# Performance work log

Hardware: AMD Instinct MI355X
Metric: run time of the kernel (lower is better)

## Reference

```python
import jax, jax.numpy as jnp
import numpy as np

N = 50000   # nodes
E = 800000  # edges (avg degree 16)
IN = 128    # in_feats
D = 64      # h_feats
H = 4       # n_heads
NEG_SLOPE = 0.2  # DGL GATConv default leaky_relu slope
L = 3       # n_layers (conv_hs)


def setup_inputs() -> dict:
    key = jax.random.key(0)
    ks = jax.random.split(key, 16)
    s = 0.05
    inp = {
        "in_feat": jax.random.normal(ks[0], (N, IN), jnp.float32),
        "src": jax.random.randint(ks[1], (E,), 0, N),
        "dst": jax.random.randint(ks[2], (E,), 0, N),
        # conv1 params (DGL GATConv: fc no bias, attn_l/attn_r, output bias)
        "W1": jax.random.normal(ks[3], (IN, H * D), jnp.float32) * s,
        "al1": jax.random.normal(ks[4], (H, D), jnp.float32) * s,
        "ar1": jax.random.normal(ks[5], (H, D), jnp.float32) * s,
        "b1": jnp.zeros((H * D,), jnp.float32),
        # stacked hidden GATConv params (L layers)
        "Wh": jax.random.normal(ks[6], (L, D, H * D), jnp.float32) * s,
        "alh": jax.random.normal(ks[7], (L, H, D), jnp.float32) * s,
        "arh": jax.random.normal(ks[8], (L, H, D), jnp.float32) * s,
        "bh": jnp.zeros((L, H * D), jnp.float32),
        # out_ln: Linear(H*D -> D)
        "Wo": jax.random.normal(ks[9], (H * D, D), jnp.float32) * s,
        "bo": jnp.zeros((D,), jnp.float32),
    }
    return inp


def gat_conv(h, W, al, ar, b, src, dst):
    # h: [N, F_in] -> feat: [N, H, D]
    feat = (h @ W).reshape(N, H, -1)
    el = jnp.einsum('nhd,hd->nh', feat, al)  # [N, H]
    er = jnp.einsum('nhd,hd->nh', feat, ar)  # [N, H]
    e = jax.nn.leaky_relu(el[src] + er[dst], NEG_SLOPE)  # [E, H]
    # segment softmax over incoming edges of each dst node
    emax = jax.ops.segment_max(e, dst, num_segments=N)
    emax = jnp.where(jnp.isfinite(emax), emax, 0.0)  # guard empty segments
    a = jnp.exp(e - emax[dst])
    ssum = jax.ops.segment_sum(a, dst, num_segments=N)
    alpha = a / ssum[dst]  # [E, H]
    # weighted scatter-aggregate of source features
    out = jax.ops.segment_sum(feat[src] * alpha[:, :, None], dst, num_segments=N)
    return out + b.reshape(1, H, -1)  # [N, H, D]


def reference(in_feat, src, dst, W1, al1, ar1, b1, Wh, alh, arh, bh, Wo, bo):
    h = gat_conv(in_feat, W1, al1, ar1, b1, src, dst).mean(axis=1)  # [N, D]
    for i in range(L - 1):
        h = gat_conv(h, Wh[i], alh[i], arh[i], bh[i], src, dst).mean(axis=1)
    h = gat_conv(h, Wh[L - 1], alh[L - 1], arh[L - 1], bh[L - 1], src, dst)  # [N, H, D]
    h = h.reshape(N, H * D) @ Wo + bo  # [N, D]
    # LayerNorm(elementwise_affine=False)
    mu = h.mean(axis=-1, keepdims=True)
    var = ((h - mu) ** 2).mean(axis=-1, keepdims=True)
    return (h - mu) / jnp.sqrt(var + 1e-5)
```

## Files before the change

### kernel.cpp

```cpp
#include <hip/hip_runtime.h>

#define NN 50000
#define NE 800000

__device__ __forceinline__ float wsum64(float v) {
#pragma unroll
  for (int off = 32; off; off >>= 1) v += __shfl_xor(v, off, 64);
  return v;
}
__device__ __forceinline__ float lrelu(float x) { return x > 0.0f ? x : 0.2f * x; }

__global__ void zero_int_k(int* __restrict__ p, int n) {
  int i = blockIdx.x * 256 + threadIdx.x;
  if (i < n) p[i] = 0;
}

__global__ void count_deg_k(const int* __restrict__ dst, int* __restrict__ deg) {
  int e = blockIdx.x * 256 + threadIdx.x;
  if (e < NE) atomicAdd(&deg[dst[e]], 1);
}

__global__ __launch_bounds__(1024) void scan_k(const int* __restrict__ deg,
                                               int* __restrict__ row_ptr,
                                               int* __restrict__ cursor) {
  __shared__ int woff[16];
  int tid = threadIdx.x;
  int lane = tid & 63, wv = tid >> 6;
  const int CH = (NN + 1023) / 1024;
  int lo = tid * CH;
  int hi = lo + CH;
  if (lo > NN) lo = NN;
  if (hi > NN) hi = NN;
  int s = 0;
  for (int i = lo; i < hi; ++i) s += deg[i];
  int incl = s;
#pragma unroll
  for (int off = 1; off < 64; off <<= 1) {
    int t = __shfl_up(incl, off, 64);
    if (lane >= off) incl += t;
  }
  if (lane == 63) woff[wv] = incl;
  __syncthreads();
  if (tid == 0) {
    int run = 0;
#pragma unroll
    for (int w = 0; w < 16; ++w) { int t = woff[w]; woff[w] = run; run += t; }
    row_ptr[NN] = run;
  }
  __syncthreads();
  int run = incl - s + woff[wv];
  for (int i = lo; i < hi; ++i) {
    row_ptr[i] = run;
    cursor[i] = run;
    run += deg[i];
  }
}

__global__ void fill_csr_k(const int* __restrict__ src, const int* __restrict__ dst,
                           int* __restrict__ cursor, int* __restrict__ csr_src) {
  int e = blockIdx.x * 256 + threadIdx.x;
  if (e < NE) {
    int pos = atomicAdd(&cursor[dst[e]], 1);
    csr_src[pos] = src[e];
  }
}

__global__ void compute_q_k(const float* __restrict__ W, const float* __restrict__ al,
                            const float* __restrict__ ar, float* __restrict__ Q, int KDIM) {
  int idx = blockIdx.x * 256 + threadIdx.x;
  if (idx >= KDIM * 8) return;
  int k = idx >> 3, c = idx & 7;
  int h = c & 3;
  const float* av = (c < 4 ? al : ar) + h * 64;
  const float* wrow = W + (size_t)k * 256 + h * 64;
  float s = 0.0f;
  for (int m = 0; m < 64; ++m) s += wrow[m] * av[m];
  Q[idx] = s;
}

__global__ void compute_m_k(const float* __restrict__ Wh2, const float* __restrict__ Wo,
                            float* __restrict__ M) {
  int row = blockIdx.x;
  int d = threadIdx.x;
  int h = row >> 6, k = row & 63;
  float s = 0.0f;
  for (int j = 0; j < 64; ++j)
    s += Wh2[k * 256 + h * 64 + j] * Wo[(h * 64 + j) * 64 + d];
  M[row * 64 + d] = s;
}

__global__ void compute_c_k(const float* __restrict__ bh2, const float* __restrict__ Wo,
                            const float* __restrict__ bo, float* __restrict__ cvec) {
  int d = threadIdx.x;
  if (d >= 64) return;
  float s = bo[d];
  for (int m = 0; m < 256; ++m) s += bh2[m] * Wo[m * 64 + d];
  cvec[d] = s;
}

__global__ __launch_bounds__(256) void eler_l1_k(const float* __restrict__ X,
                                                 const float* __restrict__ Q,
                                                 float* __restrict__ elp,
                                                 float* __restrict__ erp) {
  int n = __builtin_amdgcn_readfirstlane(blockIdx.x * 4 + (threadIdx.x >> 6));
  int lane = threadIdx.x & 63;
  float2 xv = *(const float2*)&X[(n << 7) + (lane << 1)];
  float4 qa0 = *(const float4*)&Q[(lane * 2) * 8];
  float4 qb0 = *(const float4*)&Q[(lane * 2) * 8 + 4];
  float4 qa1 = *(const float4*)&Q[(lane * 2 + 1) * 8];
  float4 qb1 = *(const float4*)&Q[(lane * 2 + 1) * 8 + 4];
  float p[8];
  p[0] = xv.x * qa0.x + xv.y * qa1.x; p[1] = xv.x * qa0.y + xv.y * qa1.y;
  p[2] = xv.x * qa0.z + xv.y * qa1.z; p[3] = xv.x * qa0.w + xv.y * qa1.w;
  p[4] = xv.x * qb0.x + xv.y * qb1.x; p[5] = xv.x * qb0.y + xv.y * qb1.y;
  p[6] = xv.x * qb0.z + xv.y * qb1.z; p[7] = xv.x * qb0.w + xv.y * qb1.w;
#pragma unroll
  for (int c = 0; c < 8; ++c) p[c] = wsum64(p[c]);
  if (lane == 0) {
    *(float4*)&elp[n << 2] = make_float4(p[0], p[1], p[2], p[3]);
    *(float4*)&erp[n << 2] = make_float4(p[4], p[5], p[6], p[7]);
  }
}

__global__ __launch_bounds__(256) void fused_hidden_k(
    const float* __restrict__ x, const float* __restrict__ el,
    const float* __restrict__ er, const float* __restrict__ W,
    const float* __restrict__ b, const float* __restrict__ Qn,
    const int* __restrict__ row_ptr, const int* __restrict__ csr_src,
    float* __restrict__ hout, float* __restrict__ eln, float* __restrict__ ern) {
  __shared__ float gs[4 * 4 * 256];
  int wave = threadIdx.x >> 6, lane = threadIdx.x & 63;
  int q = lane >> 4, r = lane & 15;
  int base = (blockIdx.x * 4 + wave) * 4;
  float* gw = &gs[wave * 1024];
  int r4 = r << 2;
#pragma unroll 1
  for (int t = 0; t < 4; ++t) {
    int n = __builtin_amdgcn_readfirstlane(base + t);
    int beg = row_ptr[n], end = row_ptr[n + 1];
    float erq = er[(n << 2) + q];
    float4 a = make_float4(0.f, 0.f, 0.f, 0.f);
    float sw = 0.f;
#define ESTEP(elv, xv)                      \
  do {                                      \
    float w = __expf(lrelu((elv) + erq));   \
    sw += w;                                \
    a.x = fmaf(w, (xv).x, a.x);             \
    a.y = fmaf(w, (xv).y, a.y);             \
    a.z = fmaf(w, (xv).z, a.z);             \
    a.w = fmaf(w, (xv).w, a.w);             \
  } while (0)
    int j = beg;
    for (; j + 8 <= end; j += 8) {
      int s0 = csr_src[j + 0], s1 = csr_src[j + 1];
      int s2 = csr_src[j + 2], s3 = csr_src[j + 3];
      int s4 = csr_src[j + 4], s5 = csr_src[j + 5];
      int s6 = csr_src[j + 6], s7 = csr_src[j + 7];
      float e0 = el[(s0 << 2) + q], e1 = el[(s1 << 2) + q];
      float e2 = el[(s2 << 2) + q], e3 = el[(s3 << 2) + q];
      float e4 = el[(s4 << 2) + q], e5 = el[(s5 << 2) + q];
      float e6 = el[(s6 << 2) + q], e7 = el[(s7 << 2) + q];
      float4 x0 = *(const float4*)&x[(s0 << 6) + r4];
      float4 x1 = *(const float4*)&x[(s1 << 6) + r4];
      float4 x2 = *(const float4*)&x[(s2 << 6) + r4];
      float4 x3 = *(const float4*)&x[(s3 << 6) + r4];
      float4 x4 = *(const float4*)&x[(s4 << 6) + r4];
      float4 x5 = *(const float4*)&x[(s5 << 6) + r4];
      float4 x6 = *(const float4*)&x[(s6 << 6) + r4];
      float4 x7 = *(const float4*)&x[(s7 << 6) + r4];
      ESTEP(e0, x0); ESTEP(e1, x1); ESTEP(e2, x2); ESTEP(e3, x3);
      ESTEP(e4, x4); ESTEP(e5, x5); ESTEP(e6, x6); ESTEP(e7, x7);
    }
    for (; j < end; ++j) {
      int s0 = csr_src[j];
      float e0 = el[(s0 << 2) + q];
      float4 x0 = *(const float4*)&x[(s0 << 6) + r4];
      ESTEP(e0, x0);
    }
#undef ESTEP
    float inv = sw > 0.f ? 1.0f / sw : 0.f;
    *(float4*)&gw[t * 256 + (q << 6) + r4] =
        make_float4(a.x * inv, a.y * inv, a.z * inv, a.w * inv);
  }
  float y0 = 0.f, y1 = 0.f, y2 = 0.f, y3 = 0.f;
  for (int rr = 0; rr < 256; rr += 4) {
#pragma unroll
    for (int u = 0; u < 4; ++u) {
      int row = rr + u;
      int h = row >> 6, k = row & 63;
      float sv = W[k * 256 + (h << 6) + lane];
      y0 = fmaf(gw[0 * 256 + row], sv, y0);
      y1 = fmaf(gw[1 * 256 + row], sv, y1);
      y2 = fmaf(gw[2 * 256 + row], sv, y2);
      y3 = fmaf(gw[3 * 256 + row], sv, y3);
    }
  }
  float bsum = b[lane] + b[64 + lane] + b[128 + lane] + b[192 + lane];
  float4 qa = *(const float4*)&Qn[lane * 8];
  float4 qb = *(const float4*)&Qn[lane * 8 + 4];
  float ys[4] = {y0, y1, y2, y3};
#pragma unroll
  for (int t = 0; t < 4; ++t) {
    int n = base + t;
    float yv = 0.25f * (ys[t] + bsum);
    hout[(n << 6) + lane] = yv;
    float e0 = wsum64(yv * qa.x), e1 = wsum64(yv * qa.y);
    float e2 = wsum64(yv * qa.z), e3 = wsum64(yv * qa.w);
    float r0 = wsum64(yv * qb.x), r1 = wsum64(yv * qb.y);
    float r2 = wsum64(yv * qb.z), r3 = wsum64(yv * qb.w);
    if (lane == 0) {
      *(float4*)&eln[n << 2] = make_float4(e0, e1, e2, e3);
      *(float4*)&ern[n << 2] = make_float4(r0, r1, r2, r3);
    }
  }
}

__global__ __launch_bounds__(256) void fused_l1_k(
    const float* __restrict__ x, const float* __restrict__ el,
    const float* __restrict__ er, const float* __restrict__ W,
    const float* __restrict__ b, const float* __restrict__ Qn,
    const int* __restrict__ row_ptr, const int* __restrict__ csr_src,
    float* __restrict__ hout, float* __restrict__ eln, float* __restrict__ ern) {
  __shared__ float gs[4 * 4 * 512];
  int wave = threadIdx.x >> 6, lane = threadIdx.x & 63;
  int q = lane >> 4, r = lane & 15;
  int base = (blockIdx.x * 4 + wave) * 4;
  float* gw = &gs[wave * 2048];
  int r8 = r << 3;
#pragma unroll 1
  for (int t = 0; t < 4; ++t) {
    int n = __builtin_amdgcn_readfirstlane(base + t);
    int beg = row_ptr[n], end = row_ptr[n + 1];
    float erq = er[(n << 2) + q];
    float4 aA = make_float4(0.f, 0.f, 0.f, 0.f);
    float4 aB = make_float4(0.f, 0.f, 0.f, 0.f);
    float sw = 0.f;
#define ESTEP(elv, xa, xb)                  \
  do {                                      \
    float w = __expf(lrelu((elv) + erq));   \
    sw += w;                                \
    aA.x = fmaf(w, (xa).x, aA.x);           \
    aA.y = fmaf(w, (xa).y, aA.y);           \
    aA.z = fmaf(w, (xa).z, aA.z);           \
    aA.w = fmaf(w, (xa).w, aA.w);           \
    aB.x = fmaf(w, (xb).x, aB.x);           \
    aB.y = fmaf(w, (xb).y, aB.y);           \
    aB.z = fmaf(w, (xb).z, aB.z);           \
    aB.w = fmaf(w, (xb).w, aB.w);           \
  } while (0)
    int j = beg;
    for (; j + 4 <= end; j += 4) {
      int s0 = csr_src[j + 0], s1 = csr_src[j + 1];
      int s2 = csr_src[j + 2], s3 = csr_src[j + 3];
      float e0 = el[(s0 << 2) + q], e1 = el[(s1 << 2) + q];
      float e2 = el[(s2 << 2) + q], e3 = el[(s3 << 2) + q];
      float4 xa0 = *(const float4*)&x[(s0 << 7) + r8];
      float4 xb0 = *(const float4*)&x[(s0 << 7) + r8 + 4];
      float4 xa1 = *(const float4*)&x[(s1 << 7) + r8];
      float4 xb1 = *(const float4*)&x[(s1 << 7) + r8 + 4];
      float4 xa2 = *(const float4*)&x[(s2 << 7) + r8];
      float4 xb2 = *(const float4*)&x[(s2 << 7) + r8 + 4];
      float4 xa3 = *(const float4*)&x[(s3 << 7) + r8];
      float4 xb3 = *(const float4*)&x[(s3 << 7) + r8 + 4];
      ESTEP(e0, xa0, xb0); ESTEP(e1, xa1, xb1);
      ESTEP(e2, xa2, xb2); ESTEP(e3, xa3, xb3);
    }
    for (; j < end; ++j) {
      int s0 = csr_src[j];
      float e0 = el[(s0 << 2) + q];
      float4 xa0 = *(const float4*)&x[(s0 << 7) + r8];
      float4 xb0 = *(const float4*)&x[(s0 << 7) + r8 + 4];
      ESTEP(e0, xa0, xb0);
    }
#undef ESTEP
    float inv = sw > 0.f ? 1.0f / sw : 0.f;
    *(float4*)&gw[t * 512 + (q << 7) + r8] =
        make_float4(aA.x * inv, aA.y * inv, aA.z * inv, aA.w * inv);
    *(float4*)&gw[t * 512 + (q << 7) + r8 + 4] =
        make_float4(aB.x * inv, aB.y * inv, aB.z * inv, aB.w * inv);
  }
  float y0 = 0.f, y1 = 0.f, y2 = 0.f, y3 = 0.f;
  for (int rr = 0; rr < 512; rr += 4) {
#pragma unroll
    for (int u = 0; u < 4; ++u) {
      int row = rr + u;
      int h = row >> 7, k = row & 127;
      float sv = W[k * 256 + (h << 6) + lane];
      y0 = fmaf(gw[0 * 512 + row], sv, y0);
      y1 = fmaf(gw[1 * 512 + row], sv, y1);
      y2 = fmaf(gw[2 * 512 + row], sv, y2);
      y3 = fmaf(gw[3 * 512 + row], sv, y3);
    }
  }
  float bsum = b[lane] + b[64 + lane] + b[128 + lane] + b[192 + lane];
  float4 qa = *(const float4*)&Qn[lane * 8];
  float4 qb = *(const float4*)&Qn[lane * 8 + 4];
  float ys[4] = {y0, y1, y2, y3};
#pragma unroll
  for (int t = 0; t < 4; ++t) {
    int n = base + t;
    float yv = 0.25f * (ys[t] + bsum);
    hout[(n << 6) + lane] = yv;
    float e0 = wsum64(yv * qa.x), e1 = wsum64(yv * qa.y);
    float e2 = wsum64(yv * qa.z), e3 = wsum64(yv * qa.w);
    float r0 = wsum64(yv * qb.x), r1 = wsum64(yv * qb.y);
    float r2 = wsum64(yv * qb.z), r3 = wsum64(yv * qb.w);
    if (lane == 0) {
      *(float4*)&eln[n << 2] = make_float4(e0, e1, e2, e3);
      *(float4*)&ern[n << 2] = make_float4(r0, r1, r2, r3);
    }
  }
}

__global__ __launch_bounds__(256) void fused_final_k(
    const float* __restrict__ x, const float* __restrict__ el,
    const float* __restrict__ er, const float* __restrict__ M,
    const float* __restrict__ cvec, const int* __restrict__ row_ptr,
    const int* __restrict__ csr_src, float* __restrict__ out) {
  __shared__ float gs[4 * 4 * 256];
  int wave = threadIdx.x >> 6, lane = threadIdx.x & 63;
  int q = lane >> 4, r = lane & 15;
  int base = (blockIdx.x * 4 + wave) * 4;
  float* gw = &gs[wave * 1024];
  int r4 = r << 2;
#pragma unroll 1
  for (int t = 0; t < 4; ++t) {
    int n = __builtin_amdgcn_readfirstlane(base + t);
    int beg = row_ptr[n], end = row_ptr[n + 1];
    float erq = er[(n << 2) + q];
    float4 a = make_float4(0.f, 0.f, 0.f, 0.f);
    float sw = 0.f;
#define ESTEP(elv, xv)                      \
  do {                                      \
    float w = __expf(lrelu((elv) + erq));   \
    sw += w;                                \
    a.x = fmaf(w, (xv).x, a.x);             \
    a.y = fmaf(w, (xv).y, a.y);             \
    a.z = fmaf(w, (xv).z, a.z);             \
    a.w = fmaf(w, (xv).w, a.w);             \
  } while (0)
    int j = beg;
    for (; j + 8 <= end; j += 8) {
      int s0 = csr_src[j + 0], s1 = csr_src[j + 1];
      int s2 = csr_src[j + 2], s3 = csr_src[j + 3];
      int s4 = csr_src[j + 4], s5 = csr_src[j + 5];
      int s6 = csr_src[j + 6], s7 = csr_src[j + 7];
      float e0 = el[(s0 << 2) + q], e1 = el[(s1 << 2) + q];
      float e2 = el[(s2 << 2) + q], e3 = el[(s3 << 2) + q];
      float e4 = el[(s4 << 2) + q], e5 = el[(s5 << 2) + q];
      float e6 = el[(s6 << 2) + q], e7 = el[(s7 << 2) + q];
      float4 x0 = *(const float4*)&x[(s0 << 6) + r4];
      float4 x1 = *(const float4*)&x[(s1 << 6) + r4];
      float4 x2 = *(const float4*)&x[(s2 << 6) + r4];
      float4 x3 = *(const float4*)&x[(s3 << 6) + r4];
      float4 x4 = *(const float4*)&x[(s4 << 6) + r4];
      float4 x5 = *(const float4*)&x[(s5 << 6) + r4];
      float4 x6 = *(const float4*)&x[(s6 << 6) + r4];
      float4 x7 = *(const float4*)&x[(s7 << 6) + r4];
      ESTEP(e0, x0); ESTEP(e1, x1); ESTEP(e2, x2); ESTEP(e3, x3);
      ESTEP(e4, x4); ESTEP(e5, x5); ESTEP(e6, x6); ESTEP(e7, x7);
    }
    for (; j < end; ++j) {
      int s0 = csr_src[j];
      float e0 = el[(s0 << 2) + q];
      float4 x0 = *(const float4*)&x[(s0 << 6) + r4];
      ESTEP(e0, x0);
    }
#undef ESTEP
    float inv = sw > 0.f ? 1.0f / sw : 0.f;
    *(float4*)&gw[t * 256 + (q << 6) + r4] =
        make_float4(a.x * inv, a.y * inv, a.z * inv, a.w * inv);
  }
  float y0 = 0.f, y1 = 0.f, y2 = 0.f, y3 = 0.f;
  for (int rr = 0; rr < 256; rr += 4) {
#pragma unroll
    for (int u = 0; u < 4; ++u) {
      int row = rr + u;
      float sv = M[(row << 6) + lane];
      y0 = fmaf(gw[0 * 256 + row], sv, y0);
      y1 = fmaf(gw[1 * 256 + row], sv, y1);
      y2 = fmaf(gw[2 * 256 + row], sv, y2);
      y3 = fmaf(gw[3 * 256 + row], sv, y3);
    }
  }
  float cl = cvec[lane];
  float ys[4] = {y0 + cl, y1 + cl, y2 + cl, y3 + cl};
#pragma unroll
  for (int t = 0; t < 4; ++t) {
    int n = base + t;
    float y = ys[t];
    float mu = wsum64(y) * (1.0f / 64.0f);
    float dv = y - mu;
    float var = wsum64(dv * dv) * (1.0f / 64.0f);
    out[(n << 6) + lane] = dv * rsqrtf(var + 1e-5f);
  }
}

extern "C" void kernel_launch(void* const* d_in, const int* in_sizes, int n_in,
                              void* d_out, int out_size, void* d_ws, size_t ws_size,
                              hipStream_t stream) {
  const float* in_feat = (const float*)d_in[0];
  const int* src = (const int*)d_in[1];
  const int* dst = (const int*)d_in[2];
  const float* W1 = (const float*)d_in[3];
  const float* al1 = (const float*)d_in[4];
  const float* ar1 = (const float*)d_in[5];
  const float* b1 = (const float*)d_in[6];
  const float* Wh = (const float*)d_in[7];
  const float* alh = (const float*)d_in[8];
  const float* arh = (const float*)d_in[9];
  const float* bh = (const float*)d_in[10];
  const float* Wo = (const float*)d_in[11];
  const float* bo = (const float*)d_in[12];
  float* out = (float*)d_out;

  char* ws = (char*)d_ws;
  size_t off = 0;
  auto alloc = [&](size_t bytes) {
    void* p = ws + off;
    off = (off + bytes + 255) & ~(size_t)255;
    return p;
  };
  float* h_a = (float*)alloc((size_t)NN * 64 * 4);
  float* h_b = (float*)alloc((size_t)NN * 64 * 4);
  float* el_a = (float*)alloc((size_t)NN * 4 * 4);
  float* er_a = (float*)alloc((size_t)NN * 4 * 4);
  float* el_b = (float*)alloc((size_t)NN * 4 * 4);
  float* er_b = (float*)alloc((size_t)NN * 4 * 4);
  float* Q1 = (float*)alloc(128 * 8 * 4);
  float* Q2 = (float*)alloc(64 * 8 * 4);
  float* Q3 = (float*)alloc(64 * 8 * 4);
  float* Q4 = (float*)alloc(64 * 8 * 4);
  float* M = (float*)alloc(256 * 64 * 4);
  float* cvec = (float*)alloc(64 * 4);
  int* deg = (int*)alloc((size_t)NN * 4);
  int* row_ptr = (int*)alloc((size_t)(NN + 1) * 4);
  int* cursor = (int*)alloc((size_t)NN * 4);
  int* csr_src = (int*)alloc((size_t)NE * 4);
  (void)ws_size; (void)in_sizes; (void)n_in; (void)out_size;

  zero_int_k<<<(NN + 255) / 256, 256, 0, stream>>>(deg, NN);
  count_deg_k<<<(NE + 255) / 256, 256, 0, stream>>>(dst, deg);
  scan_k<<<1, 1024, 0, stream>>>(deg, row_ptr, cursor);
  fill_csr_k<<<(NE + 255) / 256, 256, 0, stream>>>(src, dst, cursor, csr_src);

  compute_q_k<<<4, 256, 0, stream>>>(W1, al1, ar1, Q1, 128);
  compute_q_k<<<2, 256, 0, stream>>>(Wh + 0 * 64 * 256, alh + 0 * 256, arh + 0 * 256, Q2, 64);
  compute_q_k<<<2, 256, 0, stream>>>(Wh + 1 * 64 * 256, alh + 1 * 256, arh + 1 * 256, Q3, 64);
  compute_q_k<<<2, 256, 0, stream>>>(Wh + 2 * 64 * 256, alh + 2 * 256, arh + 2 * 256, Q4, 64);
  compute_m_k<<<256, 64, 0, stream>>>(Wh + 2 * 64 * 256, Wo, M);
  compute_c_k<<<1, 64, 0, stream>>>(bh + 2 * 256, Wo, bo, cvec);

  const int FUSED_GRID = NN / 16;
  const int ELER_GRID = NN / 4;

  eler_l1_k<<<ELER_GRID, 256, 0, stream>>>(in_feat, Q1, el_a, er_a);
  fused_l1_k<<<FUSED_GRID, 256, 0, stream>>>(in_feat, el_a, er_a, W1, b1, Q2,
                                             row_ptr, csr_src, h_a, el_b, er_b);
  fused_hidden_k<<<FUSED_GRID, 256, 0, stream>>>(h_a, el_b, er_b, Wh + 0 * 64 * 256,
                                                 bh + 0 * 256, Q3, row_ptr, csr_src,
                                                 h_b, el_a, er_a);
  fused_hidden_k<<<FUSED_GRID, 256, 0, stream>>>(h_b, el_a, er_a, Wh + 1 * 64 * 256,
                                                 bh + 1 * 256, Q4, row_ptr, csr_src,
                                                 h_a, el_b, er_b);
  fused_final_k<<<FUSED_GRID, 256, 0, stream>>>(h_a, el_b, er_b, M, cvec,
                                                row_ptr, csr_src, out);
}
```

Measured before the change: 658.3 us.

## Compute edge softmax weights per chunk in parallel and stage them in LDS

```diff
diff --git a/kernel.cpp b/kernel.cpp
--- a/kernel.cpp
+++ b/kernel.cpp
@@ -9,6 +9,7 @@
   return v;
 }
 __device__ __forceinline__ float lrelu(float x) { return x > 0.0f ? x : 0.2f * x; }
+#define RFL(v) __builtin_amdgcn_readfirstlane(v)
 
 __global__ void zero_int_k(int* __restrict__ p, int n) {
   int i = blockIdx.x * 256 + threadIdx.x;
@@ -102,7 +103,7 @@
                                                  const float* __restrict__ Q,
                                                  float* __restrict__ elp,
                                                  float* __restrict__ erp) {
-  int n = __builtin_amdgcn_readfirstlane(blockIdx.x * 4 + (threadIdx.x >> 6));
+  int n = RFL(blockIdx.x * 4 + (threadIdx.x >> 6));
   int lane = threadIdx.x & 63;
   float2 xv = *(const float2*)&X[(n << 7) + (lane << 1)];
   float4 qa0 = *(const float4*)&Q[(lane * 2) * 8];
@@ -122,65 +123,95 @@
   }
 }
 
+__device__ __forceinline__ void weights_chunk(const float* __restrict__ el,
+                                              const float4& er4,
+                                              const int* __restrict__ csr_src,
+                                              int j0, int cnt, int lane,
+                                              int* __restrict__ s_l,
+                                              float4* __restrict__ w_l,
+                                              float& sw0, float& sw1,
+                                              float& sw2, float& sw3) {
+  float4 wv = make_float4(0.f, 0.f, 0.f, 0.f);
+  int sv = 0;
+  if (lane < cnt) {
+    sv = csr_src[j0 + lane];
+    float4 l4 = *(const float4*)&el[sv << 2];
+    wv.x = __expf(lrelu(l4.x + er4.x));
+    wv.y = __expf(lrelu(l4.y + er4.y));
+    wv.z = __expf(lrelu(l4.z + er4.z));
+    wv.w = __expf(lrelu(l4.w + er4.w));
+  }
+  s_l[lane] = sv;
+  w_l[lane] = wv;
+  sw0 += wsum64(wv.x);
+  sw1 += wsum64(wv.y);
+  sw2 += wsum64(wv.z);
+  sw3 += wsum64(wv.w);
+}
+
 __global__ __launch_bounds__(256) void fused_hidden_k(
     const float* __restrict__ x, const float* __restrict__ el,
     const float* __restrict__ er, const float* __restrict__ W,
     const float* __restrict__ b, const float* __restrict__ Qn,
     const int* __restrict__ row_ptr, const int* __restrict__ csr_src,
     float* __restrict__ hout, float* __restrict__ eln, float* __restrict__ ern) {
-  __shared__ float gs[4 * 4 * 256];
+  __shared__ float gs[4][1024];
+  __shared__ int s_lds[4][64];
+  __shared__ float4 w_lds[4][64];
   int wave = threadIdx.x >> 6, lane = threadIdx.x & 63;
-  int q = lane >> 4, r = lane & 15;
   int base = (blockIdx.x * 4 + wave) * 4;
-  float* gw = &gs[wave * 1024];
-  int r4 = r << 2;
+  float* gw = gs[wave];
+  int* s_l = s_lds[wave];
+  float4* w_l = w_lds[wave];
 #pragma unroll 1
   for (int t = 0; t < 4; ++t) {
-    int n = __builtin_amdgcn_readfirstlane(base + t);
+    int n = RFL(base + t);
     int beg = row_ptr[n], end = row_ptr[n + 1];
-    float erq = er[(n << 2) + q];
-    float4 a = make_float4(0.f, 0.f, 0.f, 0.f);
-    float sw = 0.f;
-#define ESTEP(elv, xv)                      \
-  do {                                      \
-    float w = __expf(lrelu((elv) + erq));   \
-    sw += w;                                \
-    a.x = fmaf(w, (xv).x, a.x);             \
-    a.y = fmaf(w, (xv).y, a.y);             \
-    a.z = fmaf(w, (xv).z, a.z);             \
-    a.w = fmaf(w, (xv).w, a.w);             \
+    float4 er4 = *(const float4*)&er[n << 2];
+    float a0 = 0.f, a1 = 0.f, a2 = 0.f, a3 = 0.f;
+    float sw0 = 0.f, sw1 = 0.f, sw2 = 0.f, sw3 = 0.f;
+#pragma unroll 1
+    for (int j0 = beg; j0 < end; j0 += 64) {
+      int cnt = min(64, end - j0);
+      weights_chunk(el, er4, csr_src, j0, cnt, lane, s_l, w_l, sw0, sw1, sw2, sw3);
+      int j = 0;
+      for (; j + 8 <= cnt; j += 8) {
+        int t0 = RFL(s_l[j + 0]), t1 = RFL(s_l[j + 1]);
+        int t2 = RFL(s_l[j + 2]), t3 = RFL(s_l[j + 3]);
+        int t4 = RFL(s_l[j + 4]), t5 = RFL(s_l[j + 5]);
+        int t6 = RFL(s_l[j + 6]), t7 = RFL(s_l[j + 7]);
+        float x0 = x[(t0 << 6) + lane], x1 = x[(t1 << 6) + lane];
+        float x2 = x[(t2 << 6) + lane], x3 = x[(t3 << 6) + lane];
+        float x4 = x[(t4 << 6) + lane], x5 = x[(t5 << 6) + lane];
+        float x6 = x[(t6 << 6) + lane], x7 = x[(t7 << 6) + lane];
+#define FMA4(Q, X)                                 \
+  do {                                             \
+    float4 qq = (Q);                               \
+    a0 = fmaf(qq.x, (X), a0);                      \
+    a1 = fmaf(qq.y, (X), a1);                      \
+    a2 = fmaf(qq.z, (X), a2);                      \
+    a3 = fmaf(qq.w, (X), a3);                      \
   } while (0)
-    int j = beg;
-    for (; j + 8 <= end; j += 8) {
-      int s0 = csr_src[j + 0], s1 = csr_src[j + 1];
-      int s2 = csr_src[j + 2], s3 = csr_src[j + 3];
-      int s4 = csr_src[j + 4], s5 = csr_src[j + 5];
-      int s6 = csr_src[j + 6], s7 = csr_src[j + 7];
-      float e0 = el[(s0 << 2) + q], e1 = el[(s1 << 2) + q];
-      float e2 = el[(s2 << 2) + q], e3 = el[(s3 << 2) + q];
-      float e4 = el[(s4 << 2) + q], e5 = el[(s5 << 2) + q];
-      float e6 = el[(s6 << 2) + q], e7 = el[(s7 << 2) + q];
-      float4 x0 = *(const float4*)&x[(s0 << 6) + r4];
-      float4 x1 = *(const float4*)&x[(s1 << 6) + r4];
-      float4 x2 = *(const float4*)&x[(s2 << 6) + r4];
-      float4 x3 = *(const float4*)&x[(s3 << 6) + r4];
-      float4 x4 = *(const float4*)&x[(s4 << 6) + r4];
-      float4 x5 = *(const float4*)&x[(s5 << 6) + r4];
-      float4 x6 = *(const float4*)&x[(s6 << 6) + r4];
-      float4 x7 = *(const float4*)&x[(s7 << 6) + r4];
-      ESTEP(e0, x0); ESTEP(e1, x1); ESTEP(e2, x2); ESTEP(e3, x3);
-      ESTEP(e4, x4); ESTEP(e5, x5); ESTEP(e6, x6); ESTEP(e7, x7);
-    }
-    for (; j < end; ++j) {
-      int s0 = csr_src[j];
-      float e0 = el[(s0 << 2) + q];
-      float4 x0 = *(const float4*)&x[(s0 << 6) + r4];
-      ESTEP(e0, x0);
-    }
-#undef ESTEP
-    float inv = sw > 0.f ? 1.0f / sw : 0.f;
-    *(float4*)&gw[t * 256 + (q << 6) + r4] =
-        make_float4(a.x * inv, a.y * inv, a.z * inv, a.w * inv);
+        FMA4(w_l[j + 0], x0); FMA4(w_l[j + 1], x1);
+        FMA4(w_l[j + 2], x2); FMA4(w_l[j + 3], x3);
+        FMA4(w_l[j + 4], x4); FMA4(w_l[j + 5], x5);
+        FMA4(w_l[j + 6], x6); FMA4(w_l[j + 7], x7);
+      }
+      for (; j < cnt; ++j) {
+        int t0 = RFL(s_l[j]);
+        float x0 = x[(t0 << 6) + lane];
+        FMA4(w_l[j], x0);
+      }
+#undef FMA4
+    }
+    float i0 = sw0 > 0.f ? 1.0f / sw0 : 0.f;
+    float i1 = sw1 > 0.f ? 1.0f / sw1 : 0.f;
+    float i2 = sw2 > 0.f ? 1.0f / sw2 : 0.f;
+    float i3 = sw3 > 0.f ? 1.0f / sw3 : 0.f;
+    gw[t * 256 + 0 * 64 + lane] = a0 * i0;
+    gw[t * 256 + 1 * 64 + lane] = a1 * i1;
+    gw[t * 256 + 2 * 64 + lane] = a2 * i2;
+    gw[t * 256 + 3 * 64 + lane] = a3 * i3;
   }
   float y0 = 0.f, y1 = 0.f, y2 = 0.f, y3 = 0.f;
   for (int rr = 0; rr < 256; rr += 4) {
@@ -221,63 +252,73 @@
     const float* __restrict__ b, const float* __restrict__ Qn,
     const int* __restrict__ row_ptr, const int* __restrict__ csr_src,
     float* __restrict__ hout, float* __restrict__ eln, float* __restrict__ ern) {
-  __shared__ float gs[4 * 4 * 512];
+  __shared__ float gs[4][2048];
+  __shared__ int s_lds[4][64];
+  __shared__ float4 w_lds[4][64];
   int wave = threadIdx.x >> 6, lane = threadIdx.x & 63;
-  int q = lane >> 4, r = lane & 15;
   int base = (blockIdx.x * 4 + wave) * 4;
-  float* gw = &gs[wave * 2048];
-  int r8 = r << 3;
+  float* gw = gs[wave];
+  int* s_l = s_lds[wave];
+  float4* w_l = w_lds[wave];
+  int lane2 = lane << 1;
 #pragma unroll 1
   for (int t = 0; t < 4; ++t) {
-    int n = __builtin_amdgcn_readfirstlane(base + t);
+    int n = RFL(base + t);
     int beg = row_ptr[n], end = row_ptr[n + 1];
-    float erq = er[(n << 2) + q];
-    float4 aA = make_float4(0.f, 0.f, 0.f, 0.f);
-    float4 aB = make_float4(0.f, 0.f, 0.f, 0.f);
-    float sw = 0.f;
-#define ESTEP(elv, xa, xb)                  \
-  do {                                      \
-    float w = __expf(lrelu((elv) + erq));   \
-    sw += w;                                \
-    aA.x = fmaf(w, (xa).x, aA.x);           \
-    aA.y = fmaf(w, (xa).y, aA.y);           \
-    aA.z = fmaf(w, (xa).z, aA.z);           \
-    aA.w = fmaf(w, (xa).w, aA.w);           \
-    aB.x = fmaf(w, (xb).x, aB.x);           \
-    aB.y = fmaf(w, (xb).y, aB.y);           \
-    aB.z = fmaf(w, (xb).z, aB.z);           \
-    aB.w = fmaf(w, (xb).w, aB.w);           \
+    float4 er4 = *(const float4*)&er[n << 2];
+    float a0x = 0.f, a0y = 0.f, a1x = 0.f, a1y = 0.f;
+    float a2x = 0.f, a2y = 0.f, a3x = 0.f, a3y = 0.f;
+    float sw0 = 0.f, sw1 = 0.f, sw2 = 0.f, sw3 = 0.f;
+#pragma unroll 1
+    for (int j0 = beg; j0 < end; j0 += 64) {
+      int cnt = min(64, end - j0);
+      weights_chunk(el, er4, csr_src, j0, cnt, lane, s_l, w_l, sw0, sw1, sw2, sw3);
+      int j = 0;
+      for (; j + 8 <= cnt; j += 8) {
+        int t0 = RFL(s_l[j + 0]), t1 = RFL(s_l[j + 1]);
+        int t2 = RFL(s_l[j + 2]), t3 = RFL(s_l[j + 3]);
+        int t4 = RFL(s_l[j + 4]), t5 = RFL(s_l[j + 5]);
+        int t6 = RFL(s_l[j + 6]), t7 = RFL(s_l[j + 7]);
+        float2 x0 = *(const float2*)&x[(t0 << 7) + lane2];
+        float2 x1 = *(const float2*)&x[(t1 << 7) + lane2];
+        float2 x2 = *(const float2*)&x[(t2 << 7) + lane2];
+        float2 x3 = *(const float2*)&x[(t3 << 7) + lane2];
+        float2 x4 = *(const float2*)&x[(t4 << 7) + lane2];
+        float2 x5 = *(const float2*)&x[(t5 << 7) + lane2];
+        float2 x6 = *(const float2*)&x[(t6 << 7) + lane2];
+        float2 x7 = *(const float2*)&x[(t7 << 7) + lane2];
+#define FMA8(Q, X)                                   \
+  do {                                               \
+    float4 qq = (Q);                                 \
+    a0x = fmaf(qq.x, (X).x, a0x);                    \
+    a0y = fmaf(qq.x, (X).y, a0y);                    \
+    a1x = fmaf(qq.y, (X).x, a1x);                    \
+    a1y = fmaf(qq.y, (X).y, a1y);                    \
+    a2x = fmaf(qq.z, (X).x, a2x);                    \
+    a2y = fmaf(qq.z, (X).y, a2y);                    \
+    a3x = fmaf(qq.w, (X).x, a3x);                    \
+    a3y = fmaf(qq.w, (X).y, a3y);                    \
   } while (0)
-    int j = beg;
-    for (; j + 4 <= end; j += 4) {
-      int s0 = csr_src[j + 0], s1 = csr_src[j + 1];
-      int s2 = csr_src[j + 2], s3 = csr_src[j + 3];
-      float e0 = el[(s0 << 2) + q], e1 = el[(s1 << 2) + q];
-      float e2 = el[(s2 << 2) + q], e3 = el[(s3 << 2) + q];
-      float4 xa0 = *(const float4*)&x[(s0 << 7) + r8];
-      float4 xb0 = *(const float4*)&x[(s0 << 7) + r8 + 4];
-      float4 xa1 = *(const float4*)&x[(s1 << 7) + r8];
-      float4 xb1 = *(const float4*)&x[(s1 << 7) + r8 + 4];
-      float4 xa2 = *(const float4*)&x[(s2 << 7) + r8];
-      float4 xb2 = *(const float4*)&x[(s2 << 7) + r8 + 4];
-      float4 xa3 = *(const float4*)&x[(s3 << 7) + r8];
-      float4 xb3 = *(const float4*)&x[(s3 << 7) + r8 + 4];
-      ESTEP(e0, xa0, xb0); ESTEP(e1, xa1, xb1);
-      ESTEP(e2, xa2, xb2); ESTEP(e3, xa3, xb3);
-    }
-    for (; j < end; ++j) {
-      int s0 = csr_src[j];
-      float e0 = el[(s0 << 2) + q];
-      float4 xa0 = *(const float4*)&x[(s0 << 7) + r8];
-      float4 xb0 = *(const float4*)&x[(s0 << 7) + r8 + 4];
-      ESTEP(e0, xa0, xb0);
-    }
-#undef ESTEP
-    float inv = sw > 0.f ? 1.0f / sw : 0.f;
-    *(float4*)&gw[t * 512 + (q << 7) + r8] =
-        make_float4(aA.x * inv, aA.y * inv, aA.z * inv, aA.w * inv);
-    *(float4*)&gw[t * 512 + (q << 7) + r8 + 4] =
-        make_float4(aB.x * inv, aB.y * inv, aB.z * inv, aB.w * inv);
+        FMA8(w_l[j + 0], x0); FMA8(w_l[j + 1], x1);
+        FMA8(w_l[j + 2], x2); FMA8(w_l[j + 3], x3);
+        FMA8(w_l[j + 4], x4); FMA8(w_l[j + 5], x5);
+        FMA8(w_l[j + 6], x6); FMA8(w_l[j + 7], x7);
+      }
+      for (; j < cnt; ++j) {
+        int t0 = RFL(s_l[j]);
+        float2 x0 = *(const float2*)&x[(t0 << 7) + lane2];
+        FMA8(w_l[j], x0);
+      }
+#undef FMA8
+    }
+    float i0 = sw0 > 0.f ? 1.0f / sw0 : 0.f;
+    float i1 = sw1 > 0.f ? 1.0f / sw1 : 0.f;
+    float i2 = sw2 > 0.f ? 1.0f / sw2 : 0.f;
+    float i3 = sw3 > 0.f ? 1.0f / sw3 : 0.f;
+    *(float2*)&gw[t * 512 + 0 * 128 + lane2] = make_float2(a0x * i0, a0y * i0);
+    *(float2*)&gw[t * 512 + 1 * 128 + lane2] = make_float2(a1x * i1, a1y * i1);
+    *(float2*)&gw[t * 512 + 2 * 128 + lane2] = make_float2(a2x * i2, a2y * i2);
+    *(float2*)&gw[t * 512 + 3 * 128 + lane2] = make_float2(a3x * i3, a3y * i3);
   }
   float y0 = 0.f, y1 = 0.f, y2 = 0.f, y3 = 0.f;
   for (int rr = 0; rr < 512; rr += 4) {
@@ -317,59 +358,63 @@
     const float* __restrict__ er, const float* __restrict__ M,
     const float* __restrict__ cvec, const int* __restrict__ row_ptr,
     const int* __restrict__ csr_src, float* __restrict__ out) {
-  __shared__ float gs[4 * 4 * 256];
+  __shared__ float gs[4][1024];
+  __shared__ int s_lds[4][64];
+  __shared__ float4 w_lds[4][64];
   int wave = threadIdx.x >> 6, lane = threadIdx.x & 63;
-  int q = lane >> 4, r = lane & 15;
   int base = (blockIdx.x * 4 + wave) * 4;
-  float* gw = &gs[wave * 1024];
-  int r4 = r << 2;
+  float* gw = gs[wave];
+  int* s_l = s_lds[wave];
+  float4* w_l = w_lds[wave];
 #pragma unroll 1
   for (int t = 0; t < 4; ++t) {
-    int n = __builtin_amdgcn_readfirstlane(base + t);
+    int n = RFL(base + t);
     int beg = row_ptr[n], end = row_ptr[n + 1];
-    float erq = er[(n << 2) + q];
-    float4 a = make_float4(0.f, 0.f, 0.f, 0.f);
-    float sw = 0.f;
-#define ESTEP(elv, xv)                      \
-  do {                                      \
-    float w = __expf(lrelu((elv) + erq));   \
-    sw += w;                                \
-    a.x = fmaf(w, (xv).x, a.x);             \
-    a.y = fmaf(w, (xv).y, a.y);             \
-    a.z = fmaf(w, (xv).z, a.z);             \
-    a.w = fmaf(w, (xv).w, a.w);             \
+    float4 er4 = *(const float4*)&er[n << 2];
+    float a0 = 0.f, a1 = 0.f, a2 = 0.f, a3 = 0.f;
+    float sw0 = 0.f, sw1 = 0.f, sw2 = 0.f, sw3 = 0.f;
+#pragma unroll 1
+    for (int j0 = beg; j0 < end; j0 += 64) {
+      int cnt = min(64, end - j0);
+      weights_chunk(el, er4, csr_src, j0, cnt, lane, s_l, w_l, sw0, sw1, sw2, sw3);
+      int j = 0;
+      for (; j + 8 <= cnt; j += 8) {
+        int t0 = RFL(s_l[j + 0]), t1 = RFL(s_l[j + 1]);
+        int t2 = RFL(s_l[j + 2]), t3 = RFL(s_l[j + 3]);
+        int t4 = RFL(s_l[j + 4]), t5 = RFL(s_l[j + 5]);
+        int t6 = RFL(s_l[j + 6]), t7 = RFL(s_l[j + 7]);
+        float x0 = x[(t0 << 6) + lane], x1 = x[(t1 << 6) + lane];
+        float x2 = x[(t2 << 6) + lane], x3 = x[(t3 << 6) + lane];
+        float x4 = x[(t4 << 6) + lane], x5 = x[(t5 << 6) + lane];
+        float x6 = x[(t6 << 6) + lane], x7 = x[(t7 << 6) + lane];
+#define FMA4(Q, X)                                 \
+  do {                                             \
+    float4 qq = (Q);                               \
+    a0 = fmaf(qq.x, (X), a0);                      \
+    a1 = fmaf(qq.y, (X), a1);                      \
+    a2 = fmaf(qq.z, (X), a2);                      \
+    a3 = fmaf(qq.w, (X), a3);                      \
   } while (0)
-    int j = beg;
-    for (; j + 8 <= end; j += 8) {
-      int s0 = csr_src[j + 0], s1 = csr_src[j + 1];
-      int s2 = csr_src[j + 2], s3 = csr_src[j + 3];
-      int s4 = csr_src[j + 4], s5 = csr_src[j + 5];
-      int s6 = csr_src[j + 6], s7 = csr_src[j + 7];
-      float e0 = el[(s0 << 2) + q], e1 = el[(s1 << 2) + q];
-      float e2 = el[(s2 << 2) + q], e3 = el[(s3 << 2) + q];
-      float e4 = el[(s4 << 2) + q], e5 = el[(s5 << 2) + q];
-      float e6 = el[(s6 << 2) + q], e7 = el[(s7 << 2) + q];
-      float4 x0 = *(const float4*)&x[(s0 << 6) + r4];
-      float4 x1 = *(const float4*)&x[(s1 << 6) + r4];
-      float4 x2 = *(const float4*)&x[(s2 << 6) + r4];
-      float4 x3 = *(const float4*)&x[(s3 << 6) + r4];
-      float4 x4 = *(const float4*)&x[(s4 << 6) + r4];
-      float4 x5 = *(const float4*)&x[(s5 << 6) + r4];
-      float4 x6 = *(const float4*)&x[(s6 << 6) + r4];
-      float4 x7 = *(const float4*)&x[(s7 << 6) + r4];
-      ESTEP(e0, x0); ESTEP(e1, x1); ESTEP(e2, x2); ESTEP(e3, x3);
-      ESTEP(e4, x4); ESTEP(e5, x5); ESTEP(e6, x6); ESTEP(e7, x7);
-    }
-    for (; j < end; ++j) {
-      int s0 = csr_src[j];
-      float e0 = el[(s0 << 2) + q];
-      float4 x0 = *(const float4*)&x[(s0 << 6) + r4];
-      ESTEP(e0, x0);
-    }
-#undef ESTEP
-    float inv = sw > 0.f ? 1.0f / sw : 0.f;
-    *(float4*)&gw[t * 256 + (q << 6) + r4] =
-        make_float4(a.x * inv, a.y * inv, a.z * inv, a.w * inv);
+        FMA4(w_l[j + 0], x0); FMA4(w_l[j + 1], x1);
+        FMA4(w_l[j + 2], x2); FMA4(w_l[j + 3], x3);
+        FMA4(w_l[j + 4], x4); FMA4(w_l[j + 5], x5);
+        FMA4(w_l[j + 6], x6); FMA4(w_l[j + 7], x7);
+      }
+      for (; j < cnt; ++j) {
+        int t0 = RFL(s_l[j]);
+        float x0 = x[(t0 << 6) + lane];
+        FMA4(w_l[j], x0);
+      }
+#undef FMA4
+    }
+    float i0 = sw0 > 0.f ? 1.0f / sw0 : 0.f;
+    float i1 = sw1 > 0.f ? 1.0f / sw1 : 0.f;
+    float i2 = sw2 > 0.f ? 1.0f / sw2 : 0.f;
+    float i3 = sw3 > 0.f ? 1.0f / sw3 : 0.f;
+    gw[t * 256 + 0 * 64 + lane] = a0 * i0;
+    gw[t * 256 + 1 * 64 + lane] = a1 * i1;
+    gw[t * 256 + 2 * 64 + lane] = a2 * i2;
+    gw[t * 256 + 3 * 64 + lane] = a3 * i3;
   }
   float y0 = 0.f, y1 = 0.f, y2 = 0.f, y3 = 0.f;
   for (int rr = 0; rr < 256; rr += 4) {
```

Result: slower. 679.1 us (+3.2%).
